# Performance work log

Hardware: AMD Instinct MI355X
Metric: run time of the kernel (lower is better)

Reference implementation:

```python
import jax, jax.numpy as jnp
import numpy as np

B, C, H, W = 8, 4, 384, 384


def setup_inputs() -> dict:
    key = jax.random.key(0)
    k1, k2 = jax.random.split(key)
    outputs = jax.random.normal(k1, (B, C, H, W), dtype=jnp.float32)
    targets = jax.random.randint(k2, (B, H, W), 0, C)  # every class present w.h.p.
    return {"outputs": outputs, "targets": targets}


def _edt(is_zero):
    """Exact 2D Euclidean distance transform, batched.

    is_zero: bool [B,C,H,W], True at 'feature' pixels (distance 0 there).
    Returns float32 [B,C,H,W] distance to nearest True pixel.
    Separable exact algorithm (Meijster/Felzenszwalb-Huttenlocher style):
      phase 1: 1D distance along H via forward+backward scans;
      phase 2: dt^2(x,y) = min_j g(x,j)^2 + (y-j)^2 via a scan over y.
    """
    b, c, h, w = is_zero.shape
    BIG = jnp.float32(h + w)  # finite sentinel (exceeds any true distance)

    def pass1(carry, z):
        d = jnp.where(z, jnp.float32(0.0), jnp.minimum(carry + 1.0, BIG))
        return d, d

    init = jnp.full((b, c, w), BIG, jnp.float32)
    zt = jnp.moveaxis(is_zero, 2, 0)  # [H,B,C,W]
    _, fwd = jax.lax.scan(pass1, init, zt)
    _, bwd = jax.lax.scan(pass1, init, zt[::-1])
    g = jnp.minimum(fwd, bwd[::-1])          # [H,B,C,W] vertical 1D distances
    g2 = jnp.moveaxis(g * g, 0, 2)           # [B,C,H,W]

    j = jnp.arange(w, dtype=jnp.float32)     # candidate columns

    def pass2(_, y):
        # min over j of g(x,j)^2 + (y-j)^2  -> [B,C,H]
        return 0, jnp.min(g2 + (y - j) ** 2, axis=-1)

    _, dt2 = jax.lax.scan(pass2, 0, j)       # [W,B,C,H]
    return jnp.sqrt(jnp.moveaxis(dt2, 0, 3))  # [B,C,H,W]


def reference(outputs, targets):
    num_classes = outputs.shape[1]
    # one-hot: true_hot[b,c,h,w] = (targets[b,h,w] == c)
    true_hot = targets[:, None, :, :] == jnp.arange(num_classes)[None, :, None, None]
    dt = _edt(true_hot)                                  # 0 at class pixels
    dmax = jnp.max(dt, axis=(2, 3), keepdims=True)       # per (b,c) slice max
    dist_map = jnp.where(true_hot, -dmax, dt)            # factor = -1
    # weight=None -> ones(C); weight_matrix/weight.sum() == 1/C
    loss = jax.nn.softmax(outputs, axis=1) * dist_map / jnp.float32(num_classes)
    return jnp.mean(loss)
```

## Files before the change

kernel.cpp:

```cpp
#include <hip/hip_runtime.h>

#define B 8
#define C 4
#define H 384
#define W 384
#define HW (H * W)
#define CHW (C * H * W)
#define NTOT (B * CHW)
#define BIG2 589824
#define TPI 144
#define NBLK (B * TPI)
#define LOG2E 1.44269504088896340736f

__device__ __forceinline__ int nearest2(unsigned long long m, int lx, int shl) {
    unsigned long long right = m >> lx;
    int dR = right ? (int)__builtin_ctzll(right) : 999;
    unsigned long long leftb = m << shl;
    int dL = leftb ? (int)__builtin_clzll(leftb) : 999;
    int d = min(dR, dL);
    return d * d;
}

__device__ __forceinline__ int scan32(unsigned int right, unsigned int left, int add) {
    int dR = right ? __builtin_ctz(right) : 999;
    int dL = left ? __builtin_clz(left) : 999;
    int d = min(dR, dL);
    return d * d + add;
}

__device__ __attribute__((noinline))
int ring_fallback(const int* __restrict__ tg, int xa, int ya, int c, int best) {
    for (int d = 17; d * d < best; ++d) {
        int xlo = xa - d, xhi = xa + d, ylo = ya - d, yhi = ya + d;
        for (int xx = max(xlo, 0); xx <= min(xhi, W - 1); ++xx) {
            int ddx = xx - xa;
            int bb = ddx * ddx + d * d;
            if (bb < best) {
                if (ylo >= 0 && tg[ylo * W + xx] == c) best = bb;
                if (yhi < H && tg[yhi * W + xx] == c) best = min(best, bb);
            }
        }
        for (int yy = max(ylo + 1, 0); yy <= min(yhi - 1, H - 1); ++yy) {
            int ddy = yy - ya;
            int bb = ddy * ddy + d * d;
            if (bb < best) {
                if (xlo >= 0 && tg[yy * W + xlo] == c) best = bb;
                if (xhi < W && tg[yy * W + xhi] == c) best = min(best, bb);
            }
        }
    }
    return best;
}

__global__ __launch_bounds__(256)
void dist_loss_kernel(const float* __restrict__ outputs,
                      const int* __restrict__ targets,
                      float* __restrict__ parts) {
    __shared__ unsigned long long rowsm[64][4];
    __shared__ unsigned long long big[32 * 18];
    __shared__ float sred[4][9];

    int bid = blockIdx.x;
    int bx = bid % 12, by = (bid / 12) % 12, b = bid / TPI;
    int x0 = bx * 32, y0 = by * 32;
    int tid = threadIdx.x, lane = tid & 63, wv = tid >> 6;
    const int* tg = targets + b * HW;

    bool edge = (bx == 0) | (bx == 11) | (by == 0) | (by == 11);
    if (!edge) {
        const int* tp = tg + (y0 - 16 + wv) * W + (x0 - 16 + lane);
        for (int i = 0; i < 16; ++i) {
            int r = i * 4 + wv;
            int tv = tp[i * 4 * W];
            unsigned long long m0 = __ballot(tv == 0);
            unsigned long long m1 = __ballot(tv == 1);
            unsigned long long m2 = __ballot(tv == 2);
            unsigned long long m3 = __ballot(tv == 3);
            if (lane == 0) {
                rowsm[r][0] = m0; rowsm[r][1] = m1;
                rowsm[r][2] = m2; rowsm[r][3] = m3;
            }
        }
    } else {
        for (int i = 0; i < 16; ++i) {
            int r = i * 4 + wv;
            int ya = y0 - 16 + r, xa = x0 - 16 + lane;
            bool valid = (ya >= 0) & (ya < H) & (xa >= 0) & (xa < W);
            int yc = min(max(ya, 0), H - 1), xc = min(max(xa, 0), W - 1);
            int tv = tg[yc * W + xc];
            unsigned long long m0 = __ballot(valid && tv == 0);
            unsigned long long m1 = __ballot(valid && tv == 1);
            unsigned long long m2 = __ballot(valid && tv == 2);
            unsigned long long m3 = __ballot(valid && tv == 3);
            if (lane == 0) {
                rowsm[r][0] = m0; rowsm[r][1] = m1;
                rowsm[r][2] = m2; rowsm[r][3] = m3;
            }
        }
    }
    __syncthreads();

    #pragma unroll
    for (int q = 0; q < 2; ++q) {
        int idx = tid + 256 * q;
        int yy = idx >> 4, c = (idx >> 2) & 3, lvl = idx & 3;
        unsigned long long v = (lvl == 0)
            ? rowsm[16 + yy][c]
            : (rowsm[16 + yy - lvl][c] | rowsm[16 + yy + lvl][c]);
        big[yy * 18 + c * 4 + lvl] = v;
    }
    __syncthreads();

    int xq = (tid & 7) * 4;
    int y = tid >> 3;
    int ya = y0 + y, ly = y + 16;

    float red[9];
    #pragma unroll
    for (int j = 0; j < 9; ++j) red[j] = 0.0f;

    float pr[4][4];
    {
        const float* ob = outputs + (size_t)b * CHW + (size_t)ya * W + (x0 + xq);
        float4 f[4];
        f[0] = *(const float4*)ob;
        f[1] = *(const float4*)(ob + HW);
        f[2] = *(const float4*)(ob + 2 * HW);
        f[3] = *(const float4*)(ob + 3 * HW);
        #pragma unroll
        for (int c = 0; c < 4; ++c) {
            const float* fc = (const float*)&f[c];
            #pragma unroll
            for (int p = 0; p < 4; ++p) pr[c][p] = exp2f(fc[p] * LOG2E);
        }
        #pragma unroll
        for (int p = 0; p < 4; ++p) {
            float inv = 1.0f / (pr[0][p] + pr[1][p] + pr[2][p] + pr[3][p]);
            #pragma unroll
            for (int c = 0; c < 4; ++c) pr[c][p] *= inv;
        }
    }

    #pragma unroll
    for (int c = 0; c < 4; ++c) {
        const ulonglong2* pp = (const ulonglong2*)&big[y * 18 + c * 4];
        ulonglong2 va = pp[0], vb = pp[1];
        unsigned long long r0 = va.x >> xq;
        unsigned long long r1 = va.y >> xq;
        unsigned long long r2 = vb.x >> xq;
        unsigned long long r3 = vb.y >> xq;
        unsigned int l0 = (unsigned int)r0, l1 = (unsigned int)r1;
        unsigned int l2 = (unsigned int)r2, l3 = (unsigned int)r3;
        #pragma unroll
        for (int p = 0; p < 4; ++p) {
            unsigned int w0r = (unsigned int)(r0 >> (16 + p));
            unsigned int w1r = (unsigned int)(r1 >> (16 + p));
            unsigned int w2r = (unsigned int)(r2 >> (16 + p));
            unsigned int w3r = (unsigned int)(r3 >> (16 + p));
            unsigned int w0l = l0 << (15 - p);
            unsigned int w1l = l1 << (15 - p);
            unsigned int w2l = l2 << (15 - p);
            unsigned int w3l = l3 << (15 - p);
            int best = scan32(w0r, w0l, 0);
            best = min(best, scan32(w1r, w1l, 1));
            best = min(best, scan32(w2r, w2l, 4));
            best = min(best, scan32(w3r, w3l, 9));
            if (best > 16) {
                int lx = 16 + xq + p, shl = 63 - lx;
                for (int dy = 4; dy <= 16 && dy * dy < best; ++dy) {
                    unsigned long long mm = rowsm[ly + dy][c] | rowsm[ly - dy][c];
                    if (mm) best = min(best, dy * dy + nearest2(mm, lx, shl));
                }
                if (best > 289) {
                    best = min(best, BIG2);
                    best = ring_fallback(tg, x0 + xq + p, ya, c, best);
                }
            }
            float dt = sqrtf((float)best);
            red[0] += pr[c][p] * dt;
            if (w0r & 1u) red[1 + c] += pr[c][p];
            red[5 + c] = fmaxf(red[5 + c], dt);
        }
    }

    #pragma unroll
    for (int off = 32; off > 0; off >>= 1) {
        #pragma unroll
        for (int j = 0; j < 5; ++j) red[j] += __shfl_down(red[j], off);
        #pragma unroll
        for (int j = 5; j < 9; ++j) red[j] = fmaxf(red[j], __shfl_down(red[j], off));
    }
    if (lane == 0) {
        #pragma unroll
        for (int j = 0; j < 9; ++j) sred[wv][j] = red[j];
    }
    __syncthreads();
    if (tid == 0) {
        float o[9];
        #pragma unroll
        for (int j = 0; j < 9; ++j) o[j] = sred[0][j];
        #pragma unroll
        for (int w = 1; w < 4; ++w) {
            #pragma unroll
            for (int j = 0; j < 5; ++j) o[j] += sred[w][j];
            #pragma unroll
            for (int j = 5; j < 9; ++j) o[j] = fmaxf(o[j], sred[w][j]);
        }
        #pragma unroll
        for (int j = 0; j < 9; ++j) parts[j * NBLK + bid] = o[j];
    }
}

__global__ __launch_bounds__(256)
void finalize(const float* __restrict__ parts, float* __restrict__ out) {
    __shared__ double asum[4];
    __shared__ double Tsh[32];
    __shared__ float Msh[32];
    int tid = threadIdx.x, lane = tid & 63, wv = tid >> 6;

    double a = 0.0;
    for (int i = tid; i < NBLK; i += 256) a += (double)parts[i];
    #pragma unroll
    for (int off = 32; off > 0; off >>= 1) a += __shfl_down(a, off);
    if (lane == 0) asum[wv] = a;

    for (int k = 0; k < 8; ++k) {
        int s = wv * 8 + k;
        int b = s >> 2, c = s & 3;
        double ts = 0.0;
        float ms = 0.0f;
        for (int i = lane; i < TPI; i += 64) {
            int blk = b * TPI + i;
            ts += (double)parts[(1 + c) * NBLK + blk];
            ms = fmaxf(ms, parts[(5 + c) * NBLK + blk]);
        }
        #pragma unroll
        for (int off = 32; off > 0; off >>= 1) {
            ts += __shfl_down(ts, off);
            ms = fmaxf(ms, __shfl_down(ms, off));
        }
        if (lane == 0) { Tsh[s] = ts; Msh[s] = ms; }
    }
    __syncthreads();
    if (tid == 0) {
        double A = asum[0] + asum[1] + asum[2] + asum[3];
        double st = 0.0;
        for (int s = 0; s < 32; ++s) st += (double)Msh[s] * Tsh[s];
        out[0] = (float)((A - st) / ((double)C * (double)NTOT));
    }
}

extern "C" void kernel_launch(void* const* d_in, const int* in_sizes, int n_in,
                              void* d_out, int out_size, void* d_ws, size_t ws_size,
                              hipStream_t stream) {
    const float* outputs = (const float*)d_in[0];
    const int* targets = (const int*)d_in[1];
    float* out = (float*)d_out;
    float* parts = (float*)d_ws;

    dist_loss_kernel<<<NBLK, 256, 0, stream>>>(outputs, targets, parts);
    finalize<<<1, 256, 0, stream>>>(parts, out);
}
```

Before: 93.97 us.

## Precompute per-row class bitmasks in a prepass and fuse finalize via last-block atomic

A new build_masks kernel ballots each 64-pixel row segment of targets once into per-class 64-bit masks stored in workspace. The main kernel then assembles its 64-row halo window with a few shifted 64-bit loads instead of re-reading 4096 int targets per block with ballots. The separate finalize launch is removed: each block bumps an atomic counter and the last block performs the global reduction. This trades one extra small kernel launch and a mask round-trip through memory for far less redundant target traffic, plus the fence and atomic cost of the last-block reduction.

```diff
diff --git a/kernel.cpp b/kernel.cpp
--- a/kernel.cpp
+++ b/kernel.cpp
@@ -10,6 +10,7 @@
 #define BIG2 589824
 #define TPI 144
 #define NBLK (B * TPI)
+#define NSEG (B * H * 6)
 #define LOG2E 1.44269504088896340736f
 
 __device__ __forceinline__ int nearest2(unsigned long long m, int lx, int shl) {
@@ -53,12 +54,42 @@
 }
 
 __global__ __launch_bounds__(256)
+void build_masks(const int* __restrict__ targets,
+                 unsigned long long* __restrict__ masks,
+                 unsigned int* __restrict__ ctr) {
+    if (blockIdx.x == 0 && threadIdx.x == 0) *ctr = 0u;
+    int wv = threadIdx.x >> 6, lane = threadIdx.x & 63;
+    int seg = blockIdx.x * 4 + wv;
+    if (seg >= NSEG) return;
+    int wd = seg % 6, rem = seg / 6;
+    int tv = targets[rem * W + wd * 64 + lane];
+    unsigned long long m0 = __ballot(tv == 0);
+    unsigned long long m1 = __ballot(tv == 1);
+    unsigned long long m2 = __ballot(tv == 2);
+    unsigned long long m3 = __ballot(tv == 3);
+    if (lane == 0) {
+        unsigned long long* dst = masks + (size_t)rem * 24 + wd;
+        dst[0]  = m0;
+        dst[6]  = m1;
+        dst[12] = m2;
+        dst[18] = m3;
+    }
+}
+
+__global__ __launch_bounds__(256)
 void dist_loss_kernel(const float* __restrict__ outputs,
                       const int* __restrict__ targets,
-                      float* __restrict__ parts) {
+                      const unsigned long long* __restrict__ masks,
+                      float* __restrict__ parts,
+                      unsigned int* __restrict__ ctr,
+                      float* __restrict__ out) {
     __shared__ unsigned long long rowsm[64][4];
     __shared__ unsigned long long big[32 * 18];
     __shared__ float sred[4][9];
+    __shared__ int lastFlag;
+    __shared__ double asum[4];
+    __shared__ double Tsh[32];
+    __shared__ float Msh[32];
 
     int bid = blockIdx.x;
     int bx = bid % 12, by = (bid / 12) % 12, b = bid / TPI;
@@ -66,37 +97,20 @@
     int tid = threadIdx.x, lane = tid & 63, wv = tid >> 6;
     const int* tg = targets + b * HW;
 
-    bool edge = (bx == 0) | (bx == 11) | (by == 0) | (by == 11);
-    if (!edge) {
-        const int* tp = tg + (y0 - 16 + wv) * W + (x0 - 16 + lane);
-        for (int i = 0; i < 16; ++i) {
-            int r = i * 4 + wv;
-            int tv = tp[i * 4 * W];
-            unsigned long long m0 = __ballot(tv == 0);
-            unsigned long long m1 = __ballot(tv == 1);
-            unsigned long long m2 = __ballot(tv == 2);
-            unsigned long long m3 = __ballot(tv == 3);
-            if (lane == 0) {
-                rowsm[r][0] = m0; rowsm[r][1] = m1;
-                rowsm[r][2] = m2; rowsm[r][3] = m3;
-            }
-        }
-    } else {
-        for (int i = 0; i < 16; ++i) {
-            int r = i * 4 + wv;
-            int ya = y0 - 16 + r, xa = x0 - 16 + lane;
-            bool valid = (ya >= 0) & (ya < H) & (xa >= 0) & (xa < W);
-            int yc = min(max(ya, 0), H - 1), xc = min(max(xa, 0), W - 1);
-            int tv = tg[yc * W + xc];
-            unsigned long long m0 = __ballot(valid && tv == 0);
-            unsigned long long m1 = __ballot(valid && tv == 1);
-            unsigned long long m2 = __ballot(valid && tv == 2);
-            unsigned long long m3 = __ballot(valid && tv == 3);
-            if (lane == 0) {
-                rowsm[r][0] = m0; rowsm[r][1] = m1;
-                rowsm[r][2] = m2; rowsm[r][3] = m3;
-            }
-        }
+    {
+        int r = tid >> 2, cc = tid & 3;
+        int yaS = y0 - 16 + r;
+        unsigned long long wmask = 0ull;
+        if (yaS >= 0 && yaS < H) {
+            const unsigned long long* mrow =
+                masks + ((size_t)(b * H + yaS)) * 24 + cc * 6;
+            int bitpos = x0 - 16;
+            int iw = bitpos >> 6, sh = bitpos & 63;
+            unsigned long long lo = (iw >= 0) ? mrow[iw] : 0ull;
+            unsigned long long hi = (iw + 1 < 6) ? mrow[iw + 1] : 0ull;
+            wmask = (lo >> sh) | (hi << (64 - sh));
+        }
+        rowsm[r][cc] = wmask;
     }
     __syncthreads();
 
@@ -209,14 +223,15 @@
         #pragma unroll
         for (int j = 0; j < 9; ++j) parts[j * NBLK + bid] = o[j];
     }
-}
-
-__global__ __launch_bounds__(256)
-void finalize(const float* __restrict__ parts, float* __restrict__ out) {
-    __shared__ double asum[4];
-    __shared__ double Tsh[32];
-    __shared__ float Msh[32];
-    int tid = threadIdx.x, lane = tid & 63, wv = tid >> 6;
+
+    if (tid == 0) {
+        __threadfence();
+        unsigned int v = atomicAdd(ctr, 1u);
+        lastFlag = (v == NBLK - 1);
+    }
+    __syncthreads();
+    if (!lastFlag) return;
+    __threadfence();
 
     double a = 0.0;
     for (int i = tid; i < NBLK; i += 256) a += (double)parts[i];
@@ -226,13 +241,13 @@
 
     for (int k = 0; k < 8; ++k) {
         int s = wv * 8 + k;
-        int b = s >> 2, c = s & 3;
+        int bb = s >> 2, cc = s & 3;
         double ts = 0.0;
         float ms = 0.0f;
         for (int i = lane; i < TPI; i += 64) {
-            int blk = b * TPI + i;
-            ts += (double)parts[(1 + c) * NBLK + blk];
-            ms = fmaxf(ms, parts[(5 + c) * NBLK + blk]);
+            int blk = bb * TPI + i;
+            ts += (double)parts[(1 + cc) * NBLK + blk];
+            ms = fmaxf(ms, parts[(5 + cc) * NBLK + blk]);
         }
         #pragma unroll
         for (int off = 32; off > 0; off >>= 1) {
@@ -257,7 +272,11 @@
     const int* targets = (const int*)d_in[1];
     float* out = (float*)d_out;
     float* parts = (float*)d_ws;
-
-    dist_loss_kernel<<<NBLK, 256, 0, stream>>>(outputs, targets, parts);
-    finalize<<<1, 256, 0, stream>>>(parts, out);
-}
+    unsigned int* ctr = (unsigned int*)((char*)d_ws + 48 * 1024);
+    unsigned long long* masks =
+        (unsigned long long*)((char*)d_ws + 64 * 1024);
+
+    build_masks<<<NSEG / 4, 256, 0, stream>>>(targets, masks, ctr);
+    dist_loss_kernel<<<NBLK, 256, 0, stream>>>(outputs, targets, masks,
+                                               parts, ctr, out);
+}
```

New measurement: 111.8 us. 19.0% more time.
